# Performance work log

Hardware: AMD Instinct MI355X
Metric: run time of the kernel (lower is better)

Reference implementation:

```python
import jax, jax.numpy as jnp
import numpy as np

H = 16
D = 64  # head_dim = 1024 // 16
SCALE = D ** -0.5


def setup_inputs() -> dict:
    key = jax.random.key(0)
    ks = jax.random.split(key, 12)
    B, N, C = 2, 2048, 1024
    s = C ** -0.5
    return {
        "hidden_states": jax.random.normal(ks[0], (B, N, C), jnp.float32),
        "pos_embeds": jax.random.normal(ks[1], (B, N, C), jnp.float32),
        "Wq": jax.random.normal(ks[2], (C, C), jnp.float32) * s,
        "bq": jnp.zeros((C,), jnp.float32),
        "Wk": jax.random.normal(ks[3], (C, C), jnp.float32) * s,
        "bk": jnp.zeros((C,), jnp.float32),
        "Wv": jax.random.normal(ks[4], (C, C), jnp.float32) * s,
        "bv": jnp.zeros((C,), jnp.float32),
        "Wpos": jax.random.normal(ks[5], (C, C), jnp.float32) * s,
        "pos_bias_u": jax.random.normal(ks[6], (H, D), jnp.float32) * 0.1,
        "pos_bias_v": jax.random.normal(ks[7], (H, D), jnp.float32) * 0.1,
        "Wo": jax.random.normal(ks[8], (C, C), jnp.float32) * s,
        "bo": jnp.zeros((C,), jnp.float32),
    }


def reference(hidden_states, pos_embeds, Wq, bq, Wk, bk, Wv, bv, Wpos,
              pos_bias_u, pos_bias_v, Wo, bo):
    B, N, C = hidden_states.shape
    # projections (torch Linear: y = x @ W.T + b), split heads -> (B, N, H, D)
    q = (hidden_states @ Wq.T + bq).reshape(B, N, H, D)
    k = (hidden_states @ Wk.T + bk).reshape(B, N, H, D)
    v = (hidden_states @ Wv.T + bv).reshape(B, N, H, D)
    p = (pos_embeds @ Wpos.T).reshape(B, N, H, D)
    # relative-position biased logits: matrix_ac + matrix_bd
    q_u = q + pos_bias_u  # (B,N,H,D) + (H,D)
    q_v = q + pos_bias_v
    ac = jnp.einsum('bnhd,bmhd->bhnm', q_u, k)
    bd = jnp.einsum('bnhd,bmhd->bhnm', q_v, p)
    attn = jax.nn.softmax((ac + bd) * SCALE, axis=-1)  # (B,H,N,N)
    out = jnp.einsum('bhnm,bmhd->bnhd', attn, v).reshape(B, N, C)
    return out @ Wo.T + bo
```

## Files before the change

kernel.cpp:

```cpp
#include <hip/hip_runtime.h>
#include <hip/hip_bf16.h>


typedef short bf16x8 __attribute__((ext_vector_type(8)));
typedef float f32x4 __attribute__((ext_vector_type(4)));

#define BB 2
#define NN 2048
#define CC 1024
#define HH 16
#define DD 64
#define MM (BB * NN)
#define SC2E 0.18033688f

__device__ __forceinline__ unsigned short f2bf(float f) {
    union { float f; unsigned int u; } x; x.f = f;
    unsigned int r = x.u + 0x7FFFu + ((x.u >> 16) & 1u);
    return (unsigned short)(r >> 16);
}

__device__ __forceinline__ float bf2f(unsigned short s) {
    union { unsigned int u; float f; } x; x.u = ((unsigned int)s) << 16;
    return x.f;
}

__device__ __forceinline__ unsigned int pk2(float a, float b) {
    __hip_bfloat162 h = __float22bfloat162_rn(make_float2(a, b));
    unsigned int u; __builtin_memcpy(&u, &h, 4); return u;
}

typedef __attribute__((address_space(1))) const unsigned int* gas1_t;
typedef __attribute__((address_space(3))) unsigned int* las3_t;

__device__ __forceinline__ void gload_lds16(const unsigned short* g, unsigned short* l) {
    __builtin_amdgcn_global_load_lds((gas1_t)g, (las3_t)l, 16, 0, 0);
}

struct CastArgs {
    const float* src[7];
    unsigned short* dst[7];
    int n4[7];
};
__global__ __launch_bounds__(256) void cast_all(CastArgs a) {
    const int seg = blockIdx.y;
    const int i = blockIdx.x * 256 + threadIdx.x;
    if (i >= a.n4[seg]) return;
    float4 v = ((const float4*)a.src[seg])[i];
    uint2 u;
    u.x = pk2(v.x, v.y);
    u.y = pk2(v.z, v.w);
    ((uint2*)a.dst[seg])[i] = u;
}

struct GemmBatch {
    const unsigned short* A[4];
    const unsigned short* B[4];
    unsigned short* out[4];
    const float* bias[4];
};
__global__ __launch_bounds__(256) void gemm_qkvp(GemmBatch g) {
    constexpr int K = CC;
    const int z = blockIdx.z;
    const unsigned short* __restrict__ A = g.A[z];
    const unsigned short* __restrict__ B = g.B[z];
    unsigned short* __restrict__ out = g.out[z];
    const float* __restrict__ bias = g.bias[z];

    __shared__ unsigned short As[128 * 32];
    __shared__ unsigned short Bs[128 * 32];
    const int t = threadIdx.x;
    const int w = t >> 6, lane = t & 63, l15 = lane & 15, quad = lane >> 4;
    const int m0 = blockIdx.x * 128, n0 = blockIdx.y * 128;
    const int wm = (w >> 1) * 64, wn = (w & 1) * 64;

    f32x4 acc[4][4];
#pragma unroll
    for (int i = 0; i < 4; ++i)
#pragma unroll
        for (int j = 0; j < 4; ++j)
#pragma unroll
            for (int r = 0; r < 4; ++r) acc[i][j][r] = 0.f;

    for (int kb = 0; kb < K; kb += 32) {
        __syncthreads();
#pragma unroll
        for (int j = 0; j < 2; ++j) {
            int id = j * 256 + t;
            int row = id >> 2, c4 = (id & 3) * 8;
            gload_lds16(&A[(size_t)(m0 + row) * K + kb + c4], &As[id * 8]);
            gload_lds16(&B[(size_t)(n0 + row) * K + kb + c4], &Bs[id * 8]);
        }
        __syncthreads();
        bf16x8 af[4], bfr[4];
#pragma unroll
        for (int i = 0; i < 4; ++i)
            af[i] = *(const bf16x8*)&As[(wm + i * 16 + l15) * 32 + quad * 8];
#pragma unroll
        for (int j = 0; j < 4; ++j)
            bfr[j] = *(const bf16x8*)&Bs[(wn + j * 16 + l15) * 32 + quad * 8];
#pragma unroll
        for (int i = 0; i < 4; ++i)
#pragma unroll
            for (int j = 0; j < 4; ++j)
                acc[i][j] = __builtin_amdgcn_mfma_f32_16x16x32_bf16(af[i], bfr[j], acc[i][j], 0, 0, 0);
    }

#pragma unroll
    for (int i = 0; i < 4; ++i) {
#pragma unroll
        for (int j = 0; j < 4; ++j) {
            const int col = n0 + wn + j * 16 + l15;
            const int row_base = m0 + wm + i * 16 + quad * 4;
            if (z == 0) {
                const float bc = bias[col];
#pragma unroll
                for (int r = 0; r < 4; ++r)
                    out[(size_t)(row_base + r) * CC + col] = f2bf((acc[i][j][r] + bc) * SC2E);
            } else if (z == 1) {
                const float bc = bias[col];
#pragma unroll
                for (int r = 0; r < 4; ++r)
                    out[(size_t)(row_base + r) * CC + col] = f2bf(acc[i][j][r] + bc);
            } else if (z == 2) {
                const float bc = bias[col];
                const int b = row_base >> 11, nseq = row_base & 2047;
                const int hh = col >> 6, dd = col & 63;
                union { unsigned short s[4]; uint2 u; } pk;
#pragma unroll
                for (int r = 0; r < 4; ++r) pk.s[r] = f2bf(acc[i][j][r] + bc);
                size_t idx = ((size_t)(b * HH + hh) * DD + dd) * NN + nseq;
                *(uint2*)&out[idx] = pk.u;
            } else {
#pragma unroll
                for (int r = 0; r < 4; ++r)
                    out[(size_t)(row_base + r) * CC + col] = f2bf(acc[i][j][r]);
            }
        }
    }
}

__global__ __launch_bounds__(256) void gemm_out(const unsigned short* __restrict__ A,
                                                const unsigned short* __restrict__ B,
                                                float* __restrict__ out,
                                                const float* __restrict__ bias) {
    constexpr int K = CC;
    __shared__ unsigned short As[128 * 32];
    __shared__ unsigned short Bs[128 * 32];
    const int t = threadIdx.x;
    const int w = t >> 6, lane = t & 63, l15 = lane & 15, quad = lane >> 4;
    const int m0 = blockIdx.x * 128, n0 = blockIdx.y * 128;
    const int wm = (w >> 1) * 64, wn = (w & 1) * 64;

    f32x4 acc[4][4];
#pragma unroll
    for (int i = 0; i < 4; ++i)
#pragma unroll
        for (int j = 0; j < 4; ++j)
#pragma unroll
            for (int r = 0; r < 4; ++r) acc[i][j][r] = 0.f;

    for (int kb = 0; kb < K; kb += 32) {
        __syncthreads();
#pragma unroll
        for (int j = 0; j < 2; ++j) {
            int id = j * 256 + t;
            int row = id >> 2, c4 = (id & 3) * 8;
            gload_lds16(&A[(size_t)(m0 + row) * K + kb + c4], &As[id * 8]);
            gload_lds16(&B[(size_t)(n0 + row) * K + kb + c4], &Bs[id * 8]);
        }
        __syncthreads();
        bf16x8 af[4], bfr[4];
#pragma unroll
        for (int i = 0; i < 4; ++i)
            af[i] = *(const bf16x8*)&As[(wm + i * 16 + l15) * 32 + quad * 8];
#pragma unroll
        for (int j = 0; j < 4; ++j)
            bfr[j] = *(const bf16x8*)&Bs[(wn + j * 16 + l15) * 32 + quad * 8];
#pragma unroll
        for (int i = 0; i < 4; ++i)
#pragma unroll
            for (int j = 0; j < 4; ++j)
                acc[i][j] = __builtin_amdgcn_mfma_f32_16x16x32_bf16(af[i], bfr[j], acc[i][j], 0, 0, 0);
    }

#pragma unroll
    for (int i = 0; i < 4; ++i) {
#pragma unroll
        for (int j = 0; j < 4; ++j) {
            const int col = n0 + wn + j * 16 + l15;
            const int row_base = m0 + wm + i * 16 + quad * 4;
            const float bc = bias[col];
#pragma unroll
            for (int r = 0; r < 4; ++r)
                out[(size_t)(row_base + r) * CC + col] = acc[i][j][r] + bc;
        }
    }
}

__global__ __launch_bounds__(256) void fuse_kpc(const unsigned short* __restrict__ k,
                                                const unsigned short* __restrict__ pp,
                                                const float* __restrict__ pbu,
                                                const float* __restrict__ pbv,
                                                unsigned short* __restrict__ kp,
                                                float* __restrict__ c) {
    const int gw = (blockIdx.x * 256 + threadIdx.x) >> 6;
    const int lane = threadIdx.x & 63;
    const int row = gw >> 4, h = gw & 15;
    const size_t off = (size_t)row * CC + h * 64 + lane;
    const float kv = bf2f(k[off]), pv = bf2f(pp[off]);
    kp[off] = f2bf(kv + pv);
    float val = pbu[h * 64 + lane] * kv + pbv[h * 64 + lane] * pv;
#pragma unroll
    for (int o = 1; o < 64; o <<= 1) val += __shfl_xor(val, o);
    if (lane == 0) {
        const int b = row >> 11, n = row & 2047;
        c[((size_t)(b * HH + h)) * NN + n] = val * SC2E;
    }
}

#define PST 80
__global__ __launch_bounds__(256) void attn_kernel(const unsigned short* __restrict__ q,
                                                   const unsigned short* __restrict__ kp,
                                                   const unsigned short* __restrict__ vt,
                                                   const float* __restrict__ cb,
                                                   unsigned short* __restrict__ att) {
    __shared__ unsigned short Ks[64 * 64];
    __shared__ unsigned short Vs[64 * 64];
    __shared__ unsigned short Ps[4][16 * PST];

    const int t = threadIdx.x;
    const int w = t >> 6, lane = t & 63, l15 = lane & 15, quad = lane >> 4;
    const int qt = blockIdx.x, h = blockIdx.y, b = blockIdx.z;
    const int sw = (l15 & 7) * 8;

    const int qrow = qt * 64 + w * 16 + l15;
    const size_t qoff = ((size_t)(b * NN + qrow) * HH + h) * DD;
    bf16x8 qf[2];
#pragma unroll
    for (int c2 = 0; c2 < 2; ++c2)
        qf[c2] = *(const bf16x8*)&q[qoff + c2 * 32 + quad * 8];

    f32x4 oT[4];
    float l_lane = 0.f;
#pragma unroll
    for (int db = 0; db < 4; ++db)
#pragma unroll
        for (int r = 0; r < 4; ++r) oT[db][r] = 0.f;

    const size_t kbase = (size_t)b * NN * CC + (size_t)h * DD;
    const size_t vbase = (size_t)(b * HH + h) * DD * NN;
    const size_t cbase = (size_t)(b * HH + h) * NN;

    for (int kt = 0; kt < NN / 64; ++kt) {
        __syncthreads();
#pragma unroll
        for (int j = 0; j < 2; ++j) {
            int id = j * 256 + t, row = id >> 3, c8 = id & 7;
            int gc = (c8 ^ (row & 7)) * 8;
            gload_lds16(&kp[kbase + (size_t)(kt * 64 + row) * CC + gc], &Ks[id * 8]);
            gload_lds16(&vt[vbase + (size_t)row * NN + kt * 64 + gc], &Vs[id * 8]);
        }
        __syncthreads();

        f32x4 s[4];
#pragma unroll
        for (int t4 = 0; t4 < 4; ++t4)
            s[t4] = *(const f32x4*)&cb[cbase + kt * 64 + t4 * 16 + quad * 4];
#pragma unroll
        for (int t4 = 0; t4 < 4; ++t4) {
            const int row = t4 * 16 + l15;
#pragma unroll
            for (int c2 = 0; c2 < 2; ++c2) {
                bf16x8 kf = *(const bf16x8*)&Ks[row * 64 + ((c2 * 4 + quad) * 8 ^ sw)];
                s[t4] = __builtin_amdgcn_mfma_f32_16x16x32_bf16(kf, qf[c2], s[t4], 0, 0, 0);
            }
        }

        float rs = 0.f;
#pragma unroll
        for (int t4 = 0; t4 < 4; ++t4)
#pragma unroll
            for (int r = 0; r < 4; ++r) {
                float pv = exp2f(s[t4][r]);
                s[t4][r] = pv;
                rs += pv;
            }
        l_lane += rs;
#pragma unroll
        for (int t4 = 0; t4 < 4; ++t4) {
            uint2 pk;
            pk.x = pk2(s[t4][0], s[t4][1]);
            pk.y = pk2(s[t4][2], s[t4][3]);
            *(uint2*)&Ps[w][l15 * PST + t4 * 16 + quad * 4] = pk;
        }

#pragma unroll
        for (int c2 = 0; c2 < 2; ++c2) {
            bf16x8 pf = *(const bf16x8*)&Ps[w][l15 * PST + c2 * 32 + quad * 8];
#pragma unroll
            for (int db = 0; db < 4; ++db) {
                bf16x8 vf = *(const bf16x8*)&Vs[(db * 16 + l15) * 64 + ((c2 * 4 + quad) * 8 ^ sw)];
                oT[db] = __builtin_amdgcn_mfma_f32_16x16x32_bf16(vf, pf, oT[db], 0, 0, 0);
            }
        }
    }

    float l = l_lane;
    l += __shfl_xor(l, 16);
    l += __shfl_xor(l, 32);
    const float inv = 1.f / l;
    const size_t ob = ((size_t)(b * NN + qrow) * HH + h) * DD;
#pragma unroll
    for (int db = 0; db < 4; ++db) {
        uint2 pk;
        pk.x = pk2(oT[db][0] * inv, oT[db][1] * inv);
        pk.y = pk2(oT[db][2] * inv, oT[db][3] * inv);
        *(uint2*)&att[ob + db * 16 + quad * 4] = pk;
    }
}

extern "C" void kernel_launch(void* const* d_in, const int* in_sizes, int n_in,
                              void* d_out, int out_size, void* d_ws, size_t ws_size,
                              hipStream_t stream) {
    const float* hs   = (const float*)d_in[0];
    const float* pos  = (const float*)d_in[1];
    const float* Wq   = (const float*)d_in[2];
    const float* bq   = (const float*)d_in[3];
    const float* Wk   = (const float*)d_in[4];
    const float* bk   = (const float*)d_in[5];
    const float* Wv   = (const float*)d_in[6];
    const float* bv   = (const float*)d_in[7];
    const float* Wpos = (const float*)d_in[8];
    const float* pbu  = (const float*)d_in[9];
    const float* pbv  = (const float*)d_in[10];
    const float* Wo   = (const float*)d_in[11];
    const float* bo   = (const float*)d_in[12];
    float* out = (float*)d_out;

    const size_t nHS = (size_t)MM * CC;
    const size_t nW  = (size_t)CC * CC;

    unsigned short* p = (unsigned short*)d_ws;
    unsigned short* hsb  = p;            p += nHS;
    unsigned short* posb = p;            p += nHS;
    unsigned short* wqb  = p;            p += nW;
    unsigned short* wkb  = p;            p += nW;
    unsigned short* wvb  = p;            p += nW;
    unsigned short* wpb  = p;            p += nW;
    unsigned short* wob  = p;            p += nW;
    unsigned short* qsb  = p;            p += nHS;
    unsigned short* kbf  = p;            p += nHS;
    unsigned short* pbf  = p;            p += nHS;
    unsigned short* kpb  = p;            p += nHS;
    unsigned short* vtb  = p;            p += nHS;
    float* cb = (float*)p;               p += (size_t)BB * HH * NN * 2;
    unsigned short* attb = hsb;

    CastArgs ca;
    ca.src[0] = hs;   ca.dst[0] = hsb;  ca.n4[0] = (int)(nHS / 4);
    ca.src[1] = pos;  ca.dst[1] = posb; ca.n4[1] = (int)(nHS / 4);
    ca.src[2] = Wq;   ca.dst[2] = wqb;  ca.n4[2] = (int)(nW / 4);
    ca.src[3] = Wk;   ca.dst[3] = wkb;  ca.n4[3] = (int)(nW / 4);
    ca.src[4] = Wv;   ca.dst[4] = wvb;  ca.n4[4] = (int)(nW / 4);
    ca.src[5] = Wpos; ca.dst[5] = wpb;  ca.n4[5] = (int)(nW / 4);
    ca.src[6] = Wo;   ca.dst[6] = wob;  ca.n4[6] = (int)(nW / 4);
    dim3 cgrid((unsigned)(nHS / 4 / 256), 7);
    cast_all<<<cgrid, 256, 0, stream>>>(ca);

    GemmBatch gb;
    gb.A[0] = hsb;  gb.B[0] = wqb; gb.out[0] = qsb; gb.bias[0] = bq;
    gb.A[1] = hsb;  gb.B[1] = wkb; gb.out[1] = kbf; gb.bias[1] = bk;
    gb.A[2] = hsb;  gb.B[2] = wvb; gb.out[2] = vtb; gb.bias[2] = bv;
    gb.A[3] = posb; gb.B[3] = wpb; gb.out[3] = pbf; gb.bias[3] = nullptr;
    dim3 ggrid(MM / 128, CC / 128, 4);
    gemm_qkvp<<<ggrid, 256, 0, stream>>>(gb);

    fuse_kpc<<<MM * HH / 4, 256, 0, stream>>>(kbf, pbf, pbu, pbv, kpb, cb);

    dim3 agrid(NN / 64, HH, BB);
    attn_kernel<<<agrid, 256, 0, stream>>>(qsb, kpb, vtb, cb, attb);

    dim3 ogrid(MM / 128, CC / 128);
    gemm_out<<<ogrid, 256, 0, stream>>>(attb, wob, out, bo);
}
```

Measured before the change: 278.7 us.

## Process two query blocks per attention wave, smaller out-GEMM tiles, LDS-transposed V stores

The attention kernel now gives each wave 32 query rows (two 16-row blocks) instead of 16, so every K and V tile loaded into LDS is reused across twice as many queries. The grid is halved, and the c-bias load is hoisted ahead of the barrier. The output GEMM switches to 128x64 tiles, doubling the block count for better CU occupancy. The V-projection epilogue now transposes through LDS so it can issue 16-byte coalesced stores instead of scattered 8-byte ones. Costs are higher register pressure in attention and fewer attention blocks available to fill the GPU.

After: 264.5 us. 1.05x faster.

```diff
diff --git a/kernel.cpp b/kernel.cpp
--- a/kernel.cpp
+++ b/kernel.cpp
@@ -60,14 +60,15 @@
 };
 __global__ __launch_bounds__(256) void gemm_qkvp(GemmBatch g) {
     constexpr int K = CC;
+    __shared__ unsigned short Sh[2 * 128 * 32];
+    unsigned short* As = Sh;
+    unsigned short* Bs = Sh + 128 * 32;
     const int z = blockIdx.z;
     const unsigned short* __restrict__ A = g.A[z];
     const unsigned short* __restrict__ B = g.B[z];
     unsigned short* __restrict__ out = g.out[z];
     const float* __restrict__ bias = g.bias[z];
 
-    __shared__ unsigned short As[128 * 32];
-    __shared__ unsigned short Bs[128 * 32];
     const int t = threadIdx.x;
     const int w = t >> 6, lane = t & 63, l15 = lane & 15, quad = lane >> 4;
     const int m0 = blockIdx.x * 128, n0 = blockIdx.y * 128;
@@ -105,94 +106,44 @@
                 acc[i][j] = __builtin_amdgcn_mfma_f32_16x16x32_bf16(af[i], bfr[j], acc[i][j], 0, 0, 0);
     }
 
-#pragma unroll
-    for (int i = 0; i < 4; ++i) {
+    if (z != 2) {
+        const float sc = (z == 0) ? SC2E : 1.f;
+#pragma unroll
+        for (int i = 0; i < 4; ++i)
+#pragma unroll
+            for (int j = 0; j < 4; ++j) {
+                const int col = n0 + wn + j * 16 + l15;
+                const int row_base = m0 + wm + i * 16 + quad * 4;
+                const float bc = bias ? bias[col] : 0.f;
+#pragma unroll
+                for (int r = 0; r < 4; ++r)
+                    out[(size_t)(row_base + r) * CC + col] = f2bf((acc[i][j][r] + bc) * sc);
+            }
+    } else {
+        __syncthreads();
+        unsigned short* Tr = &Sh[w * 1152];
+        const int bI = (m0 + wm) >> 11, nseq0 = (m0 + wm) & 2047;
+        const int colL = lane >> 3;
+        const int mL = (lane & 7) * 8;
 #pragma unroll
         for (int j = 0; j < 4; ++j) {
             const int col = n0 + wn + j * 16 + l15;
-            const int row_base = m0 + wm + i * 16 + quad * 4;
-            if (z == 0) {
-                const float bc = bias[col];
-#pragma unroll
-                for (int r = 0; r < 4; ++r)
-                    out[(size_t)(row_base + r) * CC + col] = f2bf((acc[i][j][r] + bc) * SC2E);
-            } else if (z == 1) {
-                const float bc = bias[col];
-#pragma unroll
-                for (int r = 0; r < 4; ++r)
-                    out[(size_t)(row_base + r) * CC + col] = f2bf(acc[i][j][r] + bc);
-            } else if (z == 2) {
-                const float bc = bias[col];
-                const int b = row_base >> 11, nseq = row_base & 2047;
-                const int hh = col >> 6, dd = col & 63;
-                union { unsigned short s[4]; uint2 u; } pk;
-#pragma unroll
-                for (int r = 0; r < 4; ++r) pk.s[r] = f2bf(acc[i][j][r] + bc);
-                size_t idx = ((size_t)(b * HH + hh) * DD + dd) * NN + nseq;
-                *(uint2*)&out[idx] = pk.u;
-            } else {
-#pragma unroll
-                for (int r = 0; r < 4; ++r)
-                    out[(size_t)(row_base + r) * CC + col] = f2bf(acc[i][j][r]);
-            }
-        }
-    }
-}
-
-__global__ __launch_bounds__(256) void gemm_out(const unsigned short* __restrict__ A,
-                                                const unsigned short* __restrict__ B,
-                                                float* __restrict__ out,
-                                                const float* __restrict__ bias) {
-    constexpr int K = CC;
-    __shared__ unsigned short As[128 * 32];
-    __shared__ unsigned short Bs[128 * 32];
-    const int t = threadIdx.x;
-    const int w = t >> 6, lane = t & 63, l15 = lane & 15, quad = lane >> 4;
-    const int m0 = blockIdx.x * 128, n0 = blockIdx.y * 128;
-    const int wm = (w >> 1) * 64, wn = (w & 1) * 64;
-
-    f32x4 acc[4][4];
-#pragma unroll
-    for (int i = 0; i < 4; ++i)
-#pragma unroll
-        for (int j = 0; j < 4; ++j)
-#pragma unroll
-            for (int r = 0; r < 4; ++r) acc[i][j][r] = 0.f;
-
-    for (int kb = 0; kb < K; kb += 32) {
-        __syncthreads();
-#pragma unroll
-        for (int j = 0; j < 2; ++j) {
-            int id = j * 256 + t;
-            int row = id >> 2, c4 = (id & 3) * 8;
-            gload_lds16(&A[(size_t)(m0 + row) * K + kb + c4], &As[id * 8]);
-            gload_lds16(&B[(size_t)(n0 + row) * K + kb + c4], &Bs[id * 8]);
-        }
-        __syncthreads();
-        bf16x8 af[4], bfr[4];
-#pragma unroll
-        for (int i = 0; i < 4; ++i)
-            af[i] = *(const bf16x8*)&As[(wm + i * 16 + l15) * 32 + quad * 8];
-#pragma unroll
-        for (int j = 0; j < 4; ++j)
-            bfr[j] = *(const bf16x8*)&Bs[(wn + j * 16 + l15) * 32 + quad * 8];
-#pragma unroll
-        for (int i = 0; i < 4; ++i)
-#pragma unroll
-            for (int j = 0; j < 4; ++j)
-                acc[i][j] = __builtin_amdgcn_mfma_f32_16x16x32_bf16(af[i], bfr[j], acc[i][j], 0, 0, 0);
-    }
-
-#pragma unroll
-    for (int i = 0; i < 4; ++i) {
-#pragma unroll
-        for (int j = 0; j < 4; ++j) {
-            const int col = n0 + wn + j * 16 + l15;
-            const int row_base = m0 + wm + i * 16 + quad * 4;
             const float bc = bias[col];
 #pragma unroll
-            for (int r = 0; r < 4; ++r)
-                out[(size_t)(row_base + r) * CC + col] = acc[i][j][r] + bc;
+            for (int i = 0; i < 4; ++i) {
+                uint2 pk;
+                pk.x = pk2(acc[i][j][0] + bc, acc[i][j][1] + bc);
+                pk.y = pk2(acc[i][j][2] + bc, acc[i][j][3] + bc);
+                *(uint2*)&Tr[l15 * 72 + i * 16 + quad * 4] = pk;
+            }
+#pragma unroll
+            for (int p = 0; p < 2; ++p) {
+                const int cl = p * 8 + colL;
+                uint4 vv = *(const uint4*)&Tr[cl * 72 + mL];
+                const int gcol = n0 + wn + j * 16 + cl;
+                const int hh = gcol >> 6, dd = gcol & 63;
+                *(uint4*)&out[((size_t)(bI * 16 + hh) * 64 + dd) * 2048 + nseq0 + mL] = vv;
+            }
         }
     }
 }
@@ -226,32 +177,42 @@
                                                    unsigned short* __restrict__ att) {
     __shared__ unsigned short Ks[64 * 64];
     __shared__ unsigned short Vs[64 * 64];
-    __shared__ unsigned short Ps[4][16 * PST];
+    __shared__ unsigned short Ps[4][32 * PST];
 
     const int t = threadIdx.x;
     const int w = t >> 6, lane = t & 63, l15 = lane & 15, quad = lane >> 4;
     const int qt = blockIdx.x, h = blockIdx.y, b = blockIdx.z;
     const int sw = (l15 & 7) * 8;
 
-    const int qrow = qt * 64 + w * 16 + l15;
-    const size_t qoff = ((size_t)(b * NN + qrow) * HH + h) * DD;
-    bf16x8 qf[2];
-#pragma unroll
-    for (int c2 = 0; c2 < 2; ++c2)
-        qf[c2] = *(const bf16x8*)&q[qoff + c2 * 32 + quad * 8];
-
-    f32x4 oT[4];
-    float l_lane = 0.f;
+    bf16x8 qf[2][2];
+#pragma unroll
+    for (int qb = 0; qb < 2; ++qb) {
+        const int qrow = qt * 128 + w * 32 + qb * 16 + l15;
+        const size_t qoff = ((size_t)(b * NN + qrow) * HH + h) * DD;
+#pragma unroll
+        for (int c2 = 0; c2 < 2; ++c2)
+            qf[qb][c2] = *(const bf16x8*)&q[qoff + c2 * 32 + quad * 8];
+    }
+
+    f32x4 oT[4][2];
+    float l_lane[2] = {0.f, 0.f};
 #pragma unroll
     for (int db = 0; db < 4; ++db)
 #pragma unroll
-        for (int r = 0; r < 4; ++r) oT[db][r] = 0.f;
+        for (int qb = 0; qb < 2; ++qb)
+#pragma unroll
+            for (int r = 0; r < 4; ++r) oT[db][qb][r] = 0.f;
 
     const size_t kbase = (size_t)b * NN * CC + (size_t)h * DD;
     const size_t vbase = (size_t)(b * HH + h) * DD * NN;
     const size_t cbase = (size_t)(b * HH + h) * NN;
 
     for (int kt = 0; kt < NN / 64; ++kt) {
+        f32x4 c4[4];
+#pragma unroll
+        for (int t4 = 0; t4 < 4; ++t4)
+            c4[t4] = *(const f32x4*)&cb[cbase + kt * 64 + t4 * 16 + quad * 4];
+
         __syncthreads();
 #pragma unroll
         for (int j = 0; j < 2; ++j) {
@@ -262,61 +223,137 @@
         }
         __syncthreads();
 
-        f32x4 s[4];
-#pragma unroll
-        for (int t4 = 0; t4 < 4; ++t4)
-            s[t4] = *(const f32x4*)&cb[cbase + kt * 64 + t4 * 16 + quad * 4];
+        f32x4 s[2][4];
+#pragma unroll
+        for (int t4 = 0; t4 < 4; ++t4) {
+            s[0][t4] = c4[t4];
+            s[1][t4] = c4[t4];
+        }
 #pragma unroll
         for (int t4 = 0; t4 < 4; ++t4) {
             const int row = t4 * 16 + l15;
 #pragma unroll
             for (int c2 = 0; c2 < 2; ++c2) {
                 bf16x8 kf = *(const bf16x8*)&Ks[row * 64 + ((c2 * 4 + quad) * 8 ^ sw)];
-                s[t4] = __builtin_amdgcn_mfma_f32_16x16x32_bf16(kf, qf[c2], s[t4], 0, 0, 0);
-            }
-        }
-
-        float rs = 0.f;
-#pragma unroll
-        for (int t4 = 0; t4 < 4; ++t4)
-#pragma unroll
-            for (int r = 0; r < 4; ++r) {
-                float pv = exp2f(s[t4][r]);
-                s[t4][r] = pv;
-                rs += pv;
-            }
-        l_lane += rs;
-#pragma unroll
-        for (int t4 = 0; t4 < 4; ++t4) {
-            uint2 pk;
-            pk.x = pk2(s[t4][0], s[t4][1]);
-            pk.y = pk2(s[t4][2], s[t4][3]);
-            *(uint2*)&Ps[w][l15 * PST + t4 * 16 + quad * 4] = pk;
+#pragma unroll
+                for (int qb = 0; qb < 2; ++qb)
+                    s[qb][t4] = __builtin_amdgcn_mfma_f32_16x16x32_bf16(kf, qf[qb][c2], s[qb][t4], 0, 0, 0);
+            }
+        }
+
+#pragma unroll
+        for (int qb = 0; qb < 2; ++qb) {
+            float rs = 0.f;
+#pragma unroll
+            for (int t4 = 0; t4 < 4; ++t4)
+#pragma unroll
+                for (int r = 0; r < 4; ++r) {
+                    float pv = exp2f(s[qb][t4][r]);
+                    s[qb][t4][r] = pv;
+                    rs += pv;
+                }
+            l_lane[qb] += rs;
+#pragma unroll
+            for (int t4 = 0; t4 < 4; ++t4) {
+                uint2 pk;
+                pk.x = pk2(s[qb][t4][0], s[qb][t4][1]);
+                pk.y = pk2(s[qb][t4][2], s[qb][t4][3]);
+                *(uint2*)&Ps[w][(qb * 16 + l15) * PST + t4 * 16 + quad * 4] = pk;
+            }
         }
 
 #pragma unroll
         for (int c2 = 0; c2 < 2; ++c2) {
-            bf16x8 pf = *(const bf16x8*)&Ps[w][l15 * PST + c2 * 32 + quad * 8];
+            bf16x8 pf[2];
+#pragma unroll
+            for (int qb = 0; qb < 2; ++qb)
+                pf[qb] = *(const bf16x8*)&Ps[w][(qb * 16 + l15) * PST + c2 * 32 + quad * 8];
 #pragma unroll
             for (int db = 0; db < 4; ++db) {
                 bf16x8 vf = *(const bf16x8*)&Vs[(db * 16 + l15) * 64 + ((c2 * 4 + quad) * 8 ^ sw)];
-                oT[db] = __builtin_amdgcn_mfma_f32_16x16x32_bf16(vf, pf, oT[db], 0, 0, 0);
-            }
-        }
-    }
-
-    float l = l_lane;
-    l += __shfl_xor(l, 16);
-    l += __shfl_xor(l, 32);
-    const float inv = 1.f / l;
-    const size_t ob = ((size_t)(b * NN + qrow) * HH + h) * DD;
-#pragma unroll
-    for (int db = 0; db < 4; ++db) {
-        uint2 pk;
-        pk.x = pk2(oT[db][0] * inv, oT[db][1] * inv);
-        pk.y = pk2(oT[db][2] * inv, oT[db][3] * inv);
-        *(uint2*)&att[ob + db * 16 + quad * 4] = pk;
-    }
+#pragma unroll
+                for (int qb = 0; qb < 2; ++qb)
+                    oT[db][qb] = __builtin_amdgcn_mfma_f32_16x16x32_bf16(vf, pf[qb], oT[db][qb], 0, 0, 0);
+            }
+        }
+    }
+
+#pragma unroll
+    for (int qb = 0; qb < 2; ++qb) {
+        float l = l_lane[qb];
+        l += __shfl_xor(l, 16);
+        l += __shfl_xor(l, 32);
+        const float inv = 1.f / l;
+        const int qrow = qt * 128 + w * 32 + qb * 16 + l15;
+        const size_t ob = ((size_t)(b * NN + qrow) * HH + h) * DD;
+#pragma unroll
+        for (int db = 0; db < 4; ++db) {
+            uint2 pk;
+            pk.x = pk2(oT[db][qb][0] * inv, oT[db][qb][1] * inv);
+            pk.y = pk2(oT[db][qb][2] * inv, oT[db][qb][3] * inv);
+            *(uint2*)&att[ob + db * 16 + quad * 4] = pk;
+        }
+    }
+}
+
+__global__ __launch_bounds__(256) void gemm_out(const unsigned short* __restrict__ A,
+                                                const unsigned short* __restrict__ B,
+                                                float* __restrict__ out,
+                                                const float* __restrict__ bias) {
+    constexpr int K = CC;
+    __shared__ unsigned short As[128 * 32];
+    __shared__ unsigned short Bs[64 * 32];
+    const int t = threadIdx.x;
+    const int w = t >> 6, lane = t & 63, l15 = lane & 15, quad = lane >> 4;
+    const int m0 = blockIdx.x * 128, n0 = blockIdx.y * 64;
+    const int wm = (w >> 1) * 64, wn = (w & 1) * 32;
+
+    f32x4 acc[4][2];
+#pragma unroll
+    for (int i = 0; i < 4; ++i)
+#pragma unroll
+        for (int j = 0; j < 2; ++j)
+#pragma unroll
+            for (int r = 0; r < 4; ++r) acc[i][j][r] = 0.f;
+
+    for (int kb = 0; kb < K; kb += 32) {
+        __syncthreads();
+#pragma unroll
+        for (int j = 0; j < 2; ++j) {
+            int id = j * 256 + t;
+            int row = id >> 2, c4 = (id & 3) * 8;
+            gload_lds16(&A[(size_t)(m0 + row) * K + kb + c4], &As[id * 8]);
+        }
+        {
+            int row = t >> 2, c4 = (t & 3) * 8;
+            gload_lds16(&B[(size_t)(n0 + row) * K + kb + c4], &Bs[t * 8]);
+        }
+        __syncthreads();
+        bf16x8 af[4], bfr[2];
+#pragma unroll
+        for (int i = 0; i < 4; ++i)
+            af[i] = *(const bf16x8*)&As[(wm + i * 16 + l15) * 32 + quad * 8];
+#pragma unroll
+        for (int j = 0; j < 2; ++j)
+            bfr[j] = *(const bf16x8*)&Bs[(wn + j * 16 + l15) * 32 + quad * 8];
+#pragma unroll
+        for (int i = 0; i < 4; ++i)
+#pragma unroll
+            for (int j = 0; j < 2; ++j)
+                acc[i][j] = __builtin_amdgcn_mfma_f32_16x16x32_bf16(af[i], bfr[j], acc[i][j], 0, 0, 0);
+    }
+
+#pragma unroll
+    for (int i = 0; i < 4; ++i)
+#pragma unroll
+        for (int j = 0; j < 2; ++j) {
+            const int col = n0 + wn + j * 16 + l15;
+            const int row_base = m0 + wm + i * 16 + quad * 4;
+            const float bc = bias[col];
+#pragma unroll
+            for (int r = 0; r < 4; ++r)
+                out[(size_t)(row_base + r) * CC + col] = acc[i][j][r] + bc;
+        }
 }
 
 extern "C" void kernel_launch(void* const* d_in, const int* in_sizes, int n_in,
@@ -377,9 +414,9 @@
 
     fuse_kpc<<<MM * HH / 4, 256, 0, stream>>>(kbf, pbf, pbu, pbv, kpb, cb);
 
-    dim3 agrid(NN / 64, HH, BB);
+    dim3 agrid(NN / 128, HH, BB);
     attn_kernel<<<agrid, 256, 0, stream>>>(qsb, kpb, vtb, cb, attb);
 
-    dim3 ogrid(MM / 128, CC / 128);
+    dim3 ogrid(MM / 128, CC / 64);
     gemm_out<<<ogrid, 256, 0, stream>>>(attb, wob, out, bo);
 }
```
